# Kernel optimization log

Hardware: AMD Instinct MI355X
Metric: run time of the kernel (lower is better)

Reference implementation:

```python
import jax, jax.numpy as jnp
import numpy as np

B, H, N, D, S = 32, 4, 8192, 64, 3
EPS = 1e-10


def setup_inputs() -> dict:
    key = jax.random.key(0)
    ks = jax.random.split(key, 9)
    dev = 1.0 / np.sqrt(D + N)  # init scale from initialize_memory()
    memory = jax.random.uniform(ks[0], (B, N, D), minval=-dev, maxval=dev, dtype=jnp.float32)
    k = jax.random.normal(ks[1], (B, H, D), dtype=jnp.float32)
    beta = jax.random.uniform(ks[2], (B, H), dtype=jnp.float32) * 5.0          # key strength >= 0
    pw = jax.nn.softmax(jax.random.normal(ks[3], (B, H, N), dtype=jnp.float32), axis=-1)  # prev weights: simplex
    g = jax.random.uniform(ks[4], (B, H), dtype=jnp.float32)                    # gate in [0,1]
    s = jax.nn.softmax(jax.random.normal(ks[5], (B, H, S), dtype=jnp.float32), axis=-1)   # shift distribution
    gamma = 1.0 + 2.0 * jax.random.uniform(ks[6], (B, H), dtype=jnp.float32)    # sharpening >= 1
    erase = jax.random.uniform(ks[7], (B, H, D), dtype=jnp.float32)             # erase in [0,1]
    add = jax.random.normal(ks[8], (B, H, D), dtype=jnp.float32)
    return {"memory": memory, "k": k, "beta": beta, "pw": pw, "g": g,
            "s": s, "gamma": gamma, "erase": erase, "add": add}


def _ntm_step(memory, k, beta, pw, g, s, gamma, erase, add):
    # --- content addressing: softmax over slots of beta * cosine similarity ---
    kn = k / (jnp.linalg.norm(k, axis=-1, keepdims=True) + EPS)         # [B,H,D]
    mn = memory / (jnp.linalg.norm(memory, axis=-1, keepdims=True) + EPS)  # [B,N,D]
    cos = jnp.einsum('bhd,bnd->bhn', kn, mn)                            # [B,H,N]
    wc = jax.nn.softmax(beta[..., None] * cos, axis=-1)
    # --- location addressing: interpolate, circular shift, sharpen ---
    gb = g[..., None]
    wg = gb * wc + (1.0 - gb) * pw                                      # [B,H,N]
    center = (s.shape[-1] - 1) // 2
    # ws(i) = sum_j wg((i - off_j) mod N) * s(j), off_j = j - center
    ws = sum(s[..., j:j + 1] * jnp.roll(wg, j - center, axis=-1)
             for j in range(s.shape[-1]))
    wgam = ws ** gamma[..., None]
    w = wgam / jnp.sum(wgam, axis=-1, keepdims=True)                    # [B,H,N]
    # --- write: sequential erase/add outer products per head ---
    mem = memory
    for h in range(w.shape[1]):
        e = w[:, h, :, None] * erase[:, h, None, :]                     # [B,N,D]
        a = w[:, h, :, None] * add[:, h, None, :]
        mem = mem * (1.0 - e) + a
    # --- read from updated memory ---
    reading = jnp.einsum('bhn,bnd->bhd', w, mem)                        # [B,H,D]
    return reading


def reference(memory, k, beta, pw, g, s, gamma, erase, add):
    return _ntm_step(memory, k, beta, pw, g, s, gamma, erase, add)
```

## Files before the change

### kernel.cpp

```cpp
#include <hip/hip_runtime.h>
#include <math.h>

#define Bc 32
#define Hc 4
#define Nc 8192
#define Dc 64
#define EPSc 1e-10f

#define T1ROWS 256
#define NT1 (Nc / T1ROWS)
#define T2ROWS 256
#define NT2 (Nc / T2ROWS)
#define T3ROWS 128
#define NT3 (Nc / T3ROWS)

__global__ __launch_bounds__(256) void k_scores(
    const float* __restrict__ mem, const float* __restrict__ kk,
    const float* __restrict__ beta,
    float* __restrict__ tbuf, float* __restrict__ z1p)
{
    const int b = blockIdx.y, tile = blockIdx.x, tid = threadIdx.x;
    const int wave = tid >> 6, lane = tid & 63;
    const int n0 = tile * T1ROWS;

    __shared__ __align__(16) float ks[Hc][Dc];
    __shared__ float4 lrow4[T1ROWS * 8];
    __shared__ float wsum[4][Hc];

    {
        float kv = kk[(b * Hc + wave) * Dc + lane];
        float ss = kv * kv;
        #pragma unroll
        for (int off = 32; off; off >>= 1) ss += __shfl_xor(ss, off);
        float scale = beta[b * Hc + wave] / (sqrtf(ss) + EPSc);
        ks[wave][lane] = kv * scale;
    }
    __syncthreads();

    const float4* mem4 = reinterpret_cast<const float4*>(mem) + ((size_t)b * Nc + n0) * 16;

    float ssacc = 0.f;
    float dot[Hc] = {0.f, 0.f, 0.f, 0.f};

    #pragma unroll
    for (int hf = 0; hf < 2; ++hf) {
        if (hf) __syncthreads();

        #pragma unroll
        for (int k = 0; k < 8; ++k) {
            const int f = k * 256 + tid;
            const int r = f >> 3, sp = f & 7;
            const int c = sp ^ (r & 7);
            lrow4[f] = mem4[r * 16 + hf * 8 + c];
        }
        __syncthreads();

        const float4* ks4 = reinterpret_cast<const float4*>(&ks[0][0]);
        #pragma unroll
        for (int c = 0; c < 8; ++c) {
            const float4 v = lrow4[tid * 8 + (c ^ (tid & 7))];
            ssacc = fmaf(v.x, v.x, ssacc); ssacc = fmaf(v.y, v.y, ssacc);
            ssacc = fmaf(v.z, v.z, ssacc); ssacc = fmaf(v.w, v.w, ssacc);
            #pragma unroll
            for (int h = 0; h < Hc; ++h) {
                const float4 kf = ks4[h * 16 + hf * 8 + c];
                dot[h] = fmaf(v.x, kf.x, dot[h]);
                dot[h] = fmaf(v.y, kf.y, dot[h]);
                dot[h] = fmaf(v.z, kf.z, dot[h]);
                dot[h] = fmaf(v.w, kf.w, dot[h]);
            }
        }
    }

    const float inv = 1.0f / (sqrtf(ssacc) + EPSc);
    float psum[Hc];
    #pragma unroll
    for (int h = 0; h < Hc; ++h) {
        const float tv = __expf(dot[h] * inv);
        tbuf[(b * Hc + h) * Nc + n0 + tid] = tv;
        psum[h] = tv;
    }

    #pragma unroll
    for (int h = 0; h < Hc; ++h) {
        #pragma unroll
        for (int off = 32; off; off >>= 1) psum[h] += __shfl_xor(psum[h], off);
        if (lane == 0) wsum[wave][h] = psum[h];
    }
    __syncthreads();
    if (tid < Hc)
        z1p[(b * Hc + tid) * NT1 + tile] =
            wsum[0][tid] + wsum[1][tid] + wsum[2][tid] + wsum[3][tid];
}

__global__ __launch_bounds__(256) void k_shift(
    const float* __restrict__ tbuf, const float* __restrict__ z1p,
    const float* __restrict__ pw, const float* __restrict__ g,
    const float* __restrict__ s, const float* __restrict__ gamma,
    float4* __restrict__ wgbuf4, float* __restrict__ z2p,
    float* __restrict__ out)
{
    const int b = blockIdx.y, tile = blockIdx.x, tid = threadIdx.x;
    const int wave = tid >> 6, lane = tid & 63;
    const int n = tile * T2ROWS + tid;

    if (tile == 0) out[b * 256 + tid] = 0.f;

    __shared__ float invZ[Hc];
    __shared__ float gS[Hc], gmS[Hc], sS[Hc][3];
    __shared__ float wsum[4][Hc];

    {
        float v = (lane < NT1) ? z1p[(b * Hc + wave) * NT1 + lane] : 0.f;
        #pragma unroll
        for (int off = 32; off; off >>= 1) v += __shfl_xor(v, off);
        if (lane == 0) invZ[wave] = 1.0f / v;
    }
    if (tid < Hc)     { gS[tid] = g[b * Hc + tid]; gmS[tid] = gamma[b * Hc + tid]; }
    if (tid < Hc * 3) sS[tid / 3][tid % 3] = s[b * Hc * 3 + tid];
    __syncthreads();

    const int nm = (n + Nc - 1) & (Nc - 1);
    const int np = (n + 1) & (Nc - 1);

    float4 wq;
    float* wqp = reinterpret_cast<float*>(&wq);
    float psum[Hc];
    #pragma unroll
    for (int h = 0; h < Hc; ++h) {
        const int base = (b * Hc + h) * Nc;
        const float gh = gS[h], omg = 1.0f - gS[h], iz = invZ[h];
        const float wg_m = gh * tbuf[base + nm] * iz + omg * pw[base + nm];
        const float wg_c = gh * tbuf[base + n]  * iz + omg * pw[base + n];
        const float wg_p = gh * tbuf[base + np] * iz + omg * pw[base + np];
        const float wsv = sS[h][0] * wg_p + sS[h][1] * wg_c + sS[h][2] * wg_m;
        wqp[h] = __powf(wsv, gmS[h]);
        psum[h] = wqp[h];
    }
    wgbuf4[(size_t)b * Nc + n] = wq;

    #pragma unroll
    for (int h = 0; h < Hc; ++h) {
        #pragma unroll
        for (int off = 32; off; off >>= 1) psum[h] += __shfl_xor(psum[h], off);
        if (lane == 0) wsum[wave][h] = psum[h];
    }
    __syncthreads();
    if (tid < Hc)
        z2p[(b * Hc + tid) * NT2 + tile] =
            wsum[0][tid] + wsum[1][tid] + wsum[2][tid] + wsum[3][tid];
}

__global__ __launch_bounds__(256) void k_update(
    const float* __restrict__ mem, const float4* __restrict__ wgbuf4,
    const float* __restrict__ z2p, const float* __restrict__ erase,
    const float* __restrict__ add, float* __restrict__ out)
{
    const int b = blockIdx.y, tile = blockIdx.x, tid = threadIdx.x;
    const int part = tid & 15;
    const int rw   = tid >> 4;

    __shared__ float invZ2[Hc];
    {
        const int wave = tid >> 6, lane = tid & 63;
        float v = (lane < NT2) ? z2p[(b * Hc + wave) * NT2 + lane] : 0.f;
        #pragma unroll
        for (int off = 32; off; off >>= 1) v += __shfl_xor(v, off);
        if (lane == 0) invZ2[wave] = 1.0f / v;
    }
    __syncthreads();

    float4 e4[Hc], a4[Hc];
    float iz[Hc];
    #pragma unroll
    for (int h = 0; h < Hc; ++h) {
        e4[h] = *reinterpret_cast<const float4*>(erase + (b * Hc + h) * Dc + part * 4);
        a4[h] = *reinterpret_cast<const float4*>(add   + (b * Hc + h) * Dc + part * 4);
        iz[h] = invZ2[h];
    }

    float4 r4[Hc];
    #pragma unroll
    for (int h = 0; h < Hc; ++h) r4[h] = make_float4(0.f, 0.f, 0.f, 0.f);

    const int n0 = tile * T3ROWS;
    #pragma unroll 4
    for (int i = 0; i < T3ROWS / 16; ++i) {
        const int n = n0 + i * 16 + rw;
        const float4 m0 = *reinterpret_cast<const float4*>(
            mem + ((size_t)b * Nc + n) * Dc + part * 4);
        const float4 wv = wgbuf4[(size_t)b * Nc + n];
        float w[Hc];
        w[0] = wv.x * iz[0]; w[1] = wv.y * iz[1];
        w[2] = wv.z * iz[2]; w[3] = wv.w * iz[3];
        float4 m4 = m0;
        #pragma unroll
        for (int h = 0; h < Hc; ++h) {
            m4.x = m4.x * (1.0f - w[h] * e4[h].x) + w[h] * a4[h].x;
            m4.y = m4.y * (1.0f - w[h] * e4[h].y) + w[h] * a4[h].y;
            m4.z = m4.z * (1.0f - w[h] * e4[h].z) + w[h] * a4[h].z;
            m4.w = m4.w * (1.0f - w[h] * e4[h].w) + w[h] * a4[h].w;
        }
        #pragma unroll
        for (int h = 0; h < Hc; ++h) {
            r4[h].x = fmaf(w[h], m4.x, r4[h].x);
            r4[h].y = fmaf(w[h], m4.y, r4[h].y);
            r4[h].z = fmaf(w[h], m4.z, r4[h].z);
            r4[h].w = fmaf(w[h], m4.w, r4[h].w);
        }
    }

    __shared__ float4 acc[16][Hc][16];
    #pragma unroll
    for (int h = 0; h < Hc; ++h) acc[rw][h][part] = r4[h];
    __syncthreads();

    const int h = tid >> 6, d = tid & 63;
    float sum = 0.f;
    #pragma unroll
    for (int r2 = 0; r2 < 16; ++r2)
        sum += reinterpret_cast<const float*>(&acc[r2][h][d >> 2])[d & 3];
    atomicAdd(out + b * 256 + h * 64 + d, sum);
}

extern "C" void kernel_launch(void* const* d_in, const int* in_sizes, int n_in,
                              void* d_out, int out_size, void* d_ws, size_t ws_size,
                              hipStream_t stream) {
    const float* mem   = (const float*)d_in[0];
    const float* kk    = (const float*)d_in[1];
    const float* beta  = (const float*)d_in[2];
    const float* pw    = (const float*)d_in[3];
    const float* g     = (const float*)d_in[4];
    const float* s     = (const float*)d_in[5];
    const float* gamma = (const float*)d_in[6];
    const float* erase = (const float*)d_in[7];
    const float* add   = (const float*)d_in[8];
    float* out = (float*)d_out;

    float*  ws     = (float*)d_ws;
    float*  tbuf   = ws;
    float4* wgbuf4 = (float4*)(tbuf + (size_t)Bc*Hc*Nc);
    float*  z1p    = (float*)(wgbuf4 + (size_t)Bc*Nc);
    float*  z2p    = z1p + (size_t)Bc*Hc*NT1;

    k_scores<<<dim3(NT1, Bc), 256, 0, stream>>>(mem, kk, beta, tbuf, z1p);
    k_shift <<<dim3(NT2, Bc), 256, 0, stream>>>(tbuf, z1p, pw, g, s, gamma,
                                                wgbuf4, z2p, out);
    k_update<<<dim3(NT3, Bc), 256, 0, stream>>>(mem, wgbuf4, z2p, erase, add, out);
}
```

Before: 42.50 us.

## Prefetch memory halves into registers, interleave tbuf per slot, hoist loads before syncs

New measurement: 56.09 us. 32.0% more time.

```diff
diff --git a/kernel.cpp b/kernel.cpp
--- a/kernel.cpp
+++ b/kernel.cpp
@@ -17,7 +17,7 @@
 __global__ __launch_bounds__(256) void k_scores(
     const float* __restrict__ mem, const float* __restrict__ kk,
     const float* __restrict__ beta,
-    float* __restrict__ tbuf, float* __restrict__ z1p)
+    float4* __restrict__ tbuf4, float* __restrict__ z1p)
 {
     const int b = blockIdx.y, tile = blockIdx.x, tid = threadIdx.x;
     const int wave = tid >> 6, lane = tid & 63;
@@ -35,51 +35,77 @@
         float scale = beta[b * Hc + wave] / (sqrtf(ss) + EPSc);
         ks[wave][lane] = kv * scale;
     }
-    __syncthreads();
-
-    const float4* mem4 = reinterpret_cast<const float4*>(mem) + ((size_t)b * Nc + n0) * 16;
+
+    const float4* mem4 = reinterpret_cast<const float4*>(mem)
+                         + ((size_t)b * Nc + n0) * 16;
+
+    float4 rA[8];
+    #pragma unroll
+    for (int k = 0; k < 8; ++k) {
+        const int f = k * 256 + tid;
+        const int r = f >> 3, sp = f & 7, c = sp ^ (r & 7);
+        rA[k] = mem4[r * 16 + c];
+    }
+    #pragma unroll
+    for (int k = 0; k < 8; ++k) lrow4[k * 256 + tid] = rA[k];
+    __syncthreads();
+
+    float4 rB[8];
+    #pragma unroll
+    for (int k = 0; k < 8; ++k) {
+        const int f = k * 256 + tid;
+        const int r = f >> 3, sp = f & 7, c = sp ^ (r & 7);
+        rB[k] = mem4[r * 16 + 8 + c];
+    }
 
     float ssacc = 0.f;
     float dot[Hc] = {0.f, 0.f, 0.f, 0.f};
-
-    #pragma unroll
-    for (int hf = 0; hf < 2; ++hf) {
-        if (hf) __syncthreads();
-
-        #pragma unroll
-        for (int k = 0; k < 8; ++k) {
-            const int f = k * 256 + tid;
-            const int r = f >> 3, sp = f & 7;
-            const int c = sp ^ (r & 7);
-            lrow4[f] = mem4[r * 16 + hf * 8 + c];
-        }
-        __syncthreads();
-
-        const float4* ks4 = reinterpret_cast<const float4*>(&ks[0][0]);
-        #pragma unroll
-        for (int c = 0; c < 8; ++c) {
-            const float4 v = lrow4[tid * 8 + (c ^ (tid & 7))];
-            ssacc = fmaf(v.x, v.x, ssacc); ssacc = fmaf(v.y, v.y, ssacc);
-            ssacc = fmaf(v.z, v.z, ssacc); ssacc = fmaf(v.w, v.w, ssacc);
-            #pragma unroll
-            for (int h = 0; h < Hc; ++h) {
-                const float4 kf = ks4[h * 16 + hf * 8 + c];
-                dot[h] = fmaf(v.x, kf.x, dot[h]);
-                dot[h] = fmaf(v.y, kf.y, dot[h]);
-                dot[h] = fmaf(v.z, kf.z, dot[h]);
-                dot[h] = fmaf(v.w, kf.w, dot[h]);
-            }
+    const float4* ks4 = reinterpret_cast<const float4*>(&ks[0][0]);
+
+    #pragma unroll
+    for (int c = 0; c < 8; ++c) {
+        const float4 v = lrow4[tid * 8 + (c ^ (tid & 7))];
+        ssacc = fmaf(v.x, v.x, ssacc); ssacc = fmaf(v.y, v.y, ssacc);
+        ssacc = fmaf(v.z, v.z, ssacc); ssacc = fmaf(v.w, v.w, ssacc);
+        #pragma unroll
+        for (int h = 0; h < Hc; ++h) {
+            const float4 kf = ks4[h * 16 + c];
+            dot[h] = fmaf(v.x, kf.x, dot[h]);
+            dot[h] = fmaf(v.y, kf.y, dot[h]);
+            dot[h] = fmaf(v.z, kf.z, dot[h]);
+            dot[h] = fmaf(v.w, kf.w, dot[h]);
+        }
+    }
+    __syncthreads();
+    #pragma unroll
+    for (int k = 0; k < 8; ++k) lrow4[k * 256 + tid] = rB[k];
+    __syncthreads();
+
+    #pragma unroll
+    for (int c = 0; c < 8; ++c) {
+        const float4 v = lrow4[tid * 8 + (c ^ (tid & 7))];
+        ssacc = fmaf(v.x, v.x, ssacc); ssacc = fmaf(v.y, v.y, ssacc);
+        ssacc = fmaf(v.z, v.z, ssacc); ssacc = fmaf(v.w, v.w, ssacc);
+        #pragma unroll
+        for (int h = 0; h < Hc; ++h) {
+            const float4 kf = ks4[h * 16 + 8 + c];
+            dot[h] = fmaf(v.x, kf.x, dot[h]);
+            dot[h] = fmaf(v.y, kf.y, dot[h]);
+            dot[h] = fmaf(v.z, kf.z, dot[h]);
+            dot[h] = fmaf(v.w, kf.w, dot[h]);
         }
     }
 
     const float inv = 1.0f / (sqrtf(ssacc) + EPSc);
+    float4 tq;
+    float* tqp = reinterpret_cast<float*>(&tq);
     float psum[Hc];
     #pragma unroll
     for (int h = 0; h < Hc; ++h) {
-        const float tv = __expf(dot[h] * inv);
-        tbuf[(b * Hc + h) * Nc + n0 + tid] = tv;
-        psum[h] = tv;
-    }
+        tqp[h] = __expf(dot[h] * inv);
+        psum[h] = tqp[h];
+    }
+    tbuf4[(size_t)b * Nc + n0 + tid] = tq;
 
     #pragma unroll
     for (int h = 0; h < Hc; ++h) {
@@ -94,7 +120,7 @@
 }
 
 __global__ __launch_bounds__(256) void k_shift(
-    const float* __restrict__ tbuf, const float* __restrict__ z1p,
+    const float4* __restrict__ tbuf4, const float* __restrict__ z1p,
     const float* __restrict__ pw, const float* __restrict__ g,
     const float* __restrict__ s, const float* __restrict__ gamma,
     float4* __restrict__ wgbuf4, float* __restrict__ z2p,
@@ -106,6 +132,21 @@
 
     if (tile == 0) out[b * 256 + tid] = 0.f;
 
+    const int nm = (n + Nc - 1) & (Nc - 1);
+    const int np = (n + 1) & (Nc - 1);
+
+    const float4 tmv = tbuf4[(size_t)b * Nc + nm];
+    const float4 tcv = tbuf4[(size_t)b * Nc + n];
+    const float4 tpv = tbuf4[(size_t)b * Nc + np];
+    float pwm[Hc], pwc[Hc], pwp[Hc];
+    #pragma unroll
+    for (int h = 0; h < Hc; ++h) {
+        const int base = (b * Hc + h) * Nc;
+        pwm[h] = pw[base + nm];
+        pwc[h] = pw[base + n];
+        pwp[h] = pw[base + np];
+    }
+
     __shared__ float invZ[Hc];
     __shared__ float gS[Hc], gmS[Hc], sS[Hc][3];
     __shared__ float wsum[4][Hc];
@@ -120,19 +161,19 @@
     if (tid < Hc * 3) sS[tid / 3][tid % 3] = s[b * Hc * 3 + tid];
     __syncthreads();
 
-    const int nm = (n + Nc - 1) & (Nc - 1);
-    const int np = (n + 1) & (Nc - 1);
+    const float* tmf = reinterpret_cast<const float*>(&tmv);
+    const float* tcf = reinterpret_cast<const float*>(&tcv);
+    const float* tpf = reinterpret_cast<const float*>(&tpv);
 
     float4 wq;
     float* wqp = reinterpret_cast<float*>(&wq);
     float psum[Hc];
     #pragma unroll
     for (int h = 0; h < Hc; ++h) {
-        const int base = (b * Hc + h) * Nc;
         const float gh = gS[h], omg = 1.0f - gS[h], iz = invZ[h];
-        const float wg_m = gh * tbuf[base + nm] * iz + omg * pw[base + nm];
-        const float wg_c = gh * tbuf[base + n]  * iz + omg * pw[base + n];
-        const float wg_p = gh * tbuf[base + np] * iz + omg * pw[base + np];
+        const float wg_m = gh * tmf[h] * iz + omg * pwm[h];
+        const float wg_c = gh * tcf[h] * iz + omg * pwc[h];
+        const float wg_p = gh * tpf[h] * iz + omg * pwp[h];
         const float wsv = sS[h][0] * wg_p + sS[h][1] * wg_c + sS[h][2] * wg_m;
         wqp[h] = __powf(wsv, gmS[h]);
         psum[h] = wqp[h];
@@ -160,6 +201,13 @@
     const int part = tid & 15;
     const int rw   = tid >> 4;
 
+    float4 e4[Hc], a4[Hc];
+    #pragma unroll
+    for (int h = 0; h < Hc; ++h) {
+        e4[h] = *reinterpret_cast<const float4*>(erase + (b * Hc + h) * Dc + part * 4);
+        a4[h] = *reinterpret_cast<const float4*>(add   + (b * Hc + h) * Dc + part * 4);
+    }
+
     __shared__ float invZ2[Hc];
     {
         const int wave = tid >> 6, lane = tid & 63;
@@ -170,21 +218,16 @@
     }
     __syncthreads();
 
-    float4 e4[Hc], a4[Hc];
     float iz[Hc];
     #pragma unroll
-    for (int h = 0; h < Hc; ++h) {
-        e4[h] = *reinterpret_cast<const float4*>(erase + (b * Hc + h) * Dc + part * 4);
-        a4[h] = *reinterpret_cast<const float4*>(add   + (b * Hc + h) * Dc + part * 4);
-        iz[h] = invZ2[h];
-    }
+    for (int h = 0; h < Hc; ++h) iz[h] = invZ2[h];
 
     float4 r4[Hc];
     #pragma unroll
     for (int h = 0; h < Hc; ++h) r4[h] = make_float4(0.f, 0.f, 0.f, 0.f);
 
     const int n0 = tile * T3ROWS;
-    #pragma unroll 4
+    #pragma unroll
     for (int i = 0; i < T3ROWS / 16; ++i) {
         const int n = n0 + i * 16 + rw;
         const float4 m0 = *reinterpret_cast<const float4*>(
@@ -238,13 +281,13 @@
     float* out = (float*)d_out;
 
     float*  ws     = (float*)d_ws;
-    float*  tbuf   = ws;
-    float4* wgbuf4 = (float4*)(tbuf + (size_t)Bc*Hc*Nc);
-    float*  z1p    = (float*)(wgbuf4 + (size_t)Bc*Nc);
-    float*  z2p    = z1p + (size_t)Bc*Hc*NT1;
-
-    k_scores<<<dim3(NT1, Bc), 256, 0, stream>>>(mem, kk, beta, tbuf, z1p);
-    k_shift <<<dim3(NT2, Bc), 256, 0, stream>>>(tbuf, z1p, pw, g, s, gamma,
+    float4* tbuf4  = (float4*)ws;
+    float4* wgbuf4 = tbuf4 + (size_t)Bc * Nc;
+    float*  z1p    = (float*)(wgbuf4 + (size_t)Bc * Nc);
+    float*  z2p    = z1p + (size_t)Bc * Hc * NT1;
+
+    k_scores<<<dim3(NT1, Bc), 256, 0, stream>>>(mem, kk, beta, tbuf4, z1p);
+    k_shift <<<dim3(NT2, Bc), 256, 0, stream>>>(tbuf4, z1p, pw, g, s, gamma,
                                                 wgbuf4, z2p, out);
     k_update<<<dim3(NT3, Bc), 256, 0, stream>>>(mem, wgbuf4, z2p, erase, add, out);
 }
```
